# Performance work log

Hardware: AMD Instinct MI355X
Metric: run time of the kernel (lower is better)

Reference implementation:

```python
import jax, jax.numpy as jnp
import numpy as np

N = 100000
E = 1600000
F_NODE = 6
F_EDGE = 2
H = 64


def _glorot(key, shape):
    lim = float(np.sqrt(6.0 / (shape[0] + shape[1])))
    return jax.random.uniform(key, shape, jnp.float32, -lim, lim)


def setup_inputs() -> dict:
    key = jax.random.key(0)
    ks = jax.random.split(key, 16)
    inp = {
        "x": jax.random.normal(ks[0], (N, F_NODE), jnp.float32),
        "edge_index": jax.random.randint(ks[1], (2, E), 0, N, jnp.int64),
        "edge_attr": jax.random.normal(ks[2], (E, F_EDGE), jnp.float32),
        # GCN layers (PyG GCNConv: linear no-bias, then aggregate, then +bias)
        "W1": _glorot(ks[3], (F_NODE, H)), "b1": jnp.zeros((H,), jnp.float32),
        "W2": _glorot(ks[4], (H, H)), "b2": jnp.zeros((H,), jnp.float32),
        "W3": _glorot(ks[5], (H, H)), "b3": jnp.zeros((H,), jnp.float32),
        # edge_mlp
        "We1": _glorot(ks[6], (F_EDGE, H)), "be1": jnp.zeros((H,), jnp.float32),
        "We2": _glorot(ks[7], (H, H)), "be2": jnp.zeros((H,), jnp.float32),
        # predictor
        "Wp1": _glorot(ks[8], (3 * H, H)), "bp1": jnp.zeros((H,), jnp.float32),
        "Wp2": _glorot(ks[9], (H, H // 2)), "bp2": jnp.zeros((H // 2,), jnp.float32),
        "Wp3": _glorot(ks[10], (H // 2, 1)), "bp3": jnp.zeros((1,), jnp.float32),
    }
    return inp


def _gcn_conv(h, W, b, src_sl, dst_sl, norm, n):
    # PyG GCNConv with self-loops and symmetric normalization
    h = h @ W                                   # [N, H_out]
    msg = h[src_sl] * norm[:, None]             # gather + scale per edge(+loop)
    out = jax.ops.segment_sum(msg, dst_sl, num_segments=n)
    return out + b


def _forward(x, edge_attr, W1, b1, W2, b2, W3, b3, We1, be1, We2, be2,
             Wp1, bp1, Wp2, bp2, Wp3, bp3, edge_index):
    n = x.shape[0]
    src, dst = edge_index[0], edge_index[1]

    # --- edge feature injection (vectorized version of per-edge loop) ---
    ef = jax.nn.relu(edge_attr @ We1 + be1) @ We2 + be2      # [E, H]
    nef = (jax.ops.segment_sum(ef, src, num_segments=n)
           + jax.ops.segment_sum(ef, dst, num_segments=n))   # [N, H]
    ones_e = jnp.ones((ef.shape[0],), x.dtype)
    deg = (jax.ops.segment_sum(ones_e, src, num_segments=n)
           + jax.ops.segment_sum(ones_e, dst, num_segments=n))
    deg = jnp.maximum(deg, 1.0)
    nef = nef / deg[:, None]
    # hidden_dim (64) >= node feature dim (6) -> truncate
    x = x + nef[:, : x.shape[1]] * 0.5

    # --- GCN normalization with self-loops (shared across layers) ---
    loop = jnp.arange(n, dtype=src.dtype)
    src_sl = jnp.concatenate([src, loop])
    dst_sl = jnp.concatenate([dst, loop])
    deg_sl = jax.ops.segment_sum(jnp.ones_like(dst_sl, dtype=x.dtype), dst_sl,
                                 num_segments=n)
    dinv = jnp.where(deg_sl > 0, deg_sl ** -0.5, 0.0)
    norm = dinv[src_sl] * dinv[dst_sl]

    h = jax.nn.relu(_gcn_conv(x, W1, b1, src_sl, dst_sl, norm, n))
    h = jax.nn.relu(_gcn_conv(h, W2, b2, src_sl, dst_sl, norm, n))
    h = _gcn_conv(h, W3, b3, src_sl, dst_sl, norm, n)

    graph_emb = h.mean(axis=0)                 # global_mean_pool, batch=None
    node_mean = h.mean(axis=0)
    node_std = jnp.std(h, axis=0, ddof=1)      # torch.std is unbiased
    combined = jnp.concatenate([graph_emb, node_mean, node_std])  # [3H]

    p = jax.nn.relu(combined @ Wp1 + bp1)      # dropout inactive in eval
    p = jax.nn.relu(p @ Wp2 + bp2)
    out = jax.nn.sigmoid(p @ Wp3 + bp3)        # (1,)
    return out


def reference(x, edge_index, edge_attr, W1, b1, W2, b2, W3, b3,
              We1, be1, We2, be2, Wp1, bp1, Wp2, bp2, Wp3, bp3):
    return _forward(x, edge_attr, W1, b1, W2, b2, W3, b3, We1, be1, We2, be2,
                    Wp1, bp1, Wp2, bp2, Wp3, bp3, edge_index)
```

## Files before the change

kernel.cpp:

```cpp
#include <hip/hip_runtime.h>
#include <hip/hip_bf16.h>
#include <stdint.h>

typedef float floatx2 __attribute__((ext_vector_type(2)));

__device__ __forceinline__ float rdlane(float v, int l) {
    return __uint_as_float(__builtin_amdgcn_readlane(__float_as_uint(v), l));
}
__device__ __forceinline__ float bf2f(unsigned short u) {
    return __uint_as_float(((unsigned)u) << 16);
}
__device__ __forceinline__ unsigned short f2bf(float f) {
    unsigned u = __float_as_uint(f);
    u += 0x7fffu + ((u >> 16) & 1u);
    return (unsigned short)(u >> 16);
}
__device__ __forceinline__ unsigned packbf(float a, float b) {
    return (unsigned)f2bf(a) | ((unsigned)f2bf(b) << 16);
}
__device__ __forceinline__ unsigned pk_fp8x4(float a, float b, float c, float d) {
    int u = __builtin_amdgcn_cvt_pk_fp8_f32(a, b, 0, false);
    u = __builtin_amdgcn_cvt_pk_fp8_f32(c, d, u, true);
    return (unsigned)u;
}

__global__ void k_zero(int* __restrict__ cntO, int* __restrict__ cntI,
                       double* __restrict__ sums, int n) {
    int i = blockIdx.x * blockDim.x + threadIdx.x;
    if (i < 128) sums[i] = 0.0;
    if (i < n) { cntO[i] = 0; cntI[i] = 0; }
}

__global__ __launch_bounds__(256) void k_front(
    const int* __restrict__ ei, const float* __restrict__ ea,
    const float* __restrict__ We1, const float* __restrict__ be1,
    const float* __restrict__ We2, const float* __restrict__ be2,
    unsigned* __restrict__ efp, int* __restrict__ cntO, int* __restrict__ cntI,
    int* __restrict__ rankS, int* __restrict__ rankD, int E) {
    __shared__ float sWe1[128], sbe1[64], sWe2[64 * 6], sbe2[6];
    int t = threadIdx.x;
    if (t < 128) sWe1[t] = We1[t];
    if (t < 64) {
        sbe1[t] = be1[t];
#pragma unroll
        for (int c = 0; c < 6; ++c) sWe2[t * 6 + c] = We2[t * 64 + c];
    }
    if (t < 6) sbe2[t] = be2[t];
    __syncthreads();

    int e = blockIdx.x * blockDim.x + t;
    if (e >= E) return;

    int s = ei[e], d = ei[E + e];
    int rs = atomicAdd(&cntO[s], 1);
    int rd = atomicAdd(&cntI[d], 1);

    float2 aa = ((const float2*)ea)[e];
    float a0 = aa.x, a1 = aa.y;
    float acc[6];
#pragma unroll
    for (int c = 0; c < 6; ++c) acc[c] = sbe2[c];
#pragma unroll
    for (int j = 0; j < 64; ++j) {
        float h = fmaf(a0, sWe1[j], fmaf(a1, sWe1[64 + j], sbe1[j]));
        h = fmaxf(h, 0.f);
#pragma unroll
        for (int c = 0; c < 6; ++c) acc[c] = fmaf(h, sWe2[j * 6 + c], acc[c]);
    }
    unsigned* q = efp + (size_t)e * 3;
    q[0] = packbf(acc[0], acc[1]);
    q[1] = packbf(acc[2], acc[3]);
    q[2] = packbf(acc[4], acc[5]);
    rankS[e] = rs;
    rankD[e] = rd;
}

__global__ __launch_bounds__(256) void k_scan1(const int* __restrict__ cntO,
                                               const int* __restrict__ cntI,
                                               int2* __restrict__ bsum, int n) {
    __shared__ int2 l[256];
    int i = blockIdx.x * 256 + threadIdx.x;
    l[threadIdx.x] = (i < n) ? make_int2(cntO[i], cntI[i]) : make_int2(0, 0);
    __syncthreads();
    for (int s = 128; s > 0; s >>= 1) {
        if (threadIdx.x < s) {
            l[threadIdx.x].x += l[threadIdx.x + s].x;
            l[threadIdx.x].y += l[threadIdx.x + s].y;
        }
        __syncthreads();
    }
    if (threadIdx.x == 0) bsum[blockIdx.x] = l[0];
}

__global__ __launch_bounds__(512) void k_scan2(int2* __restrict__ bsum, int nb,
                                               int* __restrict__ offON,
                                               int* __restrict__ offIN) {
    __shared__ int2 l[512];
    int t = threadIdx.x;
    int2 v = (t < nb) ? bsum[t] : make_int2(0, 0);
    l[t] = v;
    __syncthreads();
    for (int s = 1; s < 512; s <<= 1) {
        int2 tmp = (t >= s) ? l[t - s] : make_int2(0, 0);
        __syncthreads();
        l[t].x += tmp.x; l[t].y += tmp.y;
        __syncthreads();
    }
    if (t < nb) bsum[t] = make_int2(l[t].x - v.x, l[t].y - v.y);
    if (t == 511) { *offON = l[511].x; *offIN = l[511].y; }
}

__global__ __launch_bounds__(256) void k_scan3off(const int* __restrict__ cntO,
                                                  const int* __restrict__ cntI,
                                                  const int2* __restrict__ bsum,
                                                  int* __restrict__ offO,
                                                  int* __restrict__ offI, int n) {
    __shared__ int2 l[256];
    int i = blockIdx.x * 256 + threadIdx.x;
    int2 v = (i < n) ? make_int2(cntO[i], cntI[i]) : make_int2(0, 0);
    l[threadIdx.x] = v;
    __syncthreads();
    for (int s = 1; s < 256; s <<= 1) {
        int2 tmp = (threadIdx.x >= (unsigned)s) ? l[threadIdx.x - s] : make_int2(0, 0);
        __syncthreads();
        l[threadIdx.x].x += tmp.x; l[threadIdx.x].y += tmp.y;
        __syncthreads();
    }
    if (i < n) {
        int2 bs = bsum[blockIdx.x];
        offO[i] = l[threadIdx.x].x - v.x + bs.x;
        offI[i] = l[threadIdx.x].y - v.y + bs.y;
    }
}

__global__ __launch_bounds__(256) void k_place(const int* __restrict__ ei,
                                               const int* __restrict__ rankS,
                                               const int* __restrict__ rankD,
                                               const int* __restrict__ offO,
                                               const int* __restrict__ offI,
                                               const unsigned* __restrict__ efp,
                                               unsigned* __restrict__ out_rec,
                                               uint4* __restrict__ in_rec, int E) {
    int e = blockIdx.x * blockDim.x + threadIdx.x;
    if (e >= E) return;
    int s = ei[e], d = ei[E + e];
    const unsigned* q = efp + (size_t)e * 3;
    unsigned u0 = q[0], u1 = q[1], u2 = q[2];
    size_t so = (size_t)(offO[s] + rankS[e]) * 3;
    out_rec[so] = u0; out_rec[so + 1] = u1; out_rec[so + 2] = u2;
    in_rec[offI[d] + rankD[e]] = make_uint4((unsigned)s, u0, u1, u2);
}

__global__ __launch_bounds__(256) void k_nef_x(
    const int* __restrict__ offO, const unsigned* __restrict__ out_rec,
    const int* __restrict__ offI, const uint4* __restrict__ in_rec,
    const float* __restrict__ x,
    float* __restrict__ xp, float* __restrict__ dinv, int n) {
    int i = blockIdx.x * blockDim.x + threadIdx.x;
    if (i >= n) return;
    int bo = offO[i], eo = offO[i + 1];
    int bi = offI[i], eiN = offI[i + 1];
    float a0 = 0.f, a1 = 0.f, a2 = 0.f, a3 = 0.f, a4 = 0.f, a5 = 0.f;
    for (int j = bo; j < eo; ++j) {
        const unsigned* q = out_rec + (size_t)j * 3;
        unsigned u0 = q[0], u1 = q[1], u2 = q[2];
        a0 += bf2f((unsigned short)u0); a1 += bf2f((unsigned short)(u0 >> 16));
        a2 += bf2f((unsigned short)u1); a3 += bf2f((unsigned short)(u1 >> 16));
        a4 += bf2f((unsigned short)u2); a5 += bf2f((unsigned short)(u2 >> 16));
    }
    for (int j = bi; j < eiN; ++j) {
        uint4 r = in_rec[j];
        a0 += bf2f((unsigned short)r.y); a1 += bf2f((unsigned short)(r.y >> 16));
        a2 += bf2f((unsigned short)r.z); a3 += bf2f((unsigned short)(r.z >> 16));
        a4 += bf2f((unsigned short)r.w); a5 += bf2f((unsigned short)(r.w >> 16));
    }
    int indeg = eiN - bi;
    float degf = (float)((eo - bo) + indeg);
    float inv = 0.5f / fmaxf(degf, 1.f);
    xp[(size_t)i * 6 + 0] = x[(size_t)i * 6 + 0] + a0 * inv;
    xp[(size_t)i * 6 + 1] = x[(size_t)i * 6 + 1] + a1 * inv;
    xp[(size_t)i * 6 + 2] = x[(size_t)i * 6 + 2] + a2 * inv;
    xp[(size_t)i * 6 + 3] = x[(size_t)i * 6 + 3] + a3 * inv;
    xp[(size_t)i * 6 + 4] = x[(size_t)i * 6 + 4] + a4 * inv;
    xp[(size_t)i * 6 + 5] = x[(size_t)i * 6 + 5] + a5 * inv;
    dinv[i] = 1.f / sqrtf(1.f + (float)indeg);
}

__global__ __launch_bounds__(256) void k_mm1(const float* __restrict__ xp,
                                             const float* __restrict__ W1,
                                             const float* __restrict__ dinv,
                                             unsigned* __restrict__ sOut, int n) {
    int lane = threadIdx.x & 63;
    int sub = lane & 15;
    int wid = (blockIdx.x * blockDim.x + threadIdx.x) >> 6;
    int nw = (gridDim.x * blockDim.x) >> 6;
    float w[6];
#pragma unroll
    for (int c = 0; c < 6; ++c) w[c] = W1[c * 64 + lane];
    for (int i = wid; i < n; i += nw) {
        float xv = (lane < 6) ? xp[(size_t)i * 6 + lane] : 0.f;
        float acc = 0.f;
#pragma unroll
        for (int c = 0; c < 6; ++c) acc = fmaf(rdlane(xv, c), w[c], acc);
        float o = acc * dinv[i];
        float o0 = __shfl(o, sub * 4 + 0);
        float o1 = __shfl(o, sub * 4 + 1);
        float o2 = __shfl(o, sub * 4 + 2);
        float o3 = __shfl(o, sub * 4 + 3);
        if (lane < 16) sOut[(size_t)i * 16 + lane] = pk_fp8x4(o0, o1, o2, o3);
    }
}

__global__ __launch_bounds__(256) void k_gathermm(
    const int* __restrict__ offI, const uint4* __restrict__ in_rec,
    const float* __restrict__ dinv, const unsigned* __restrict__ sIn,
    const float* __restrict__ bias, const float* __restrict__ W,
    unsigned* __restrict__ sOut, int n) {
    int lane = threadIdx.x & 63;
    int sub = lane & 15, grp = lane >> 4;
    int wid = (blockIdx.x * blockDim.x + threadIdx.x) >> 6;
    int nw = (gridDim.x * blockDim.x) >> 6;
    float w[64];
#pragma unroll
    for (int c = 0; c < 64; ++c) w[c] = W[c * 64 + lane];
    float4 bb = ((const float4*)bias)[sub];

    for (int i = wid; i < n; i += nw) {
        unsigned su = sIn[(size_t)i * 16 + sub];
        float a0, a1, a2, a3;
        if (grp == 0) {
            floatx2 lo = __builtin_amdgcn_cvt_pk_f32_fp8(su, false);
            floatx2 hi = __builtin_amdgcn_cvt_pk_f32_fp8(su, true);
            a0 = lo.x; a1 = lo.y; a2 = hi.x; a3 = hi.y;
        } else { a0 = a1 = a2 = a3 = 0.f; }
        int b0 = offI[i], e0 = offI[i + 1];
#pragma unroll 4
        for (int j = b0 + grp; j < e0; j += 4) {
            unsigned src = in_rec[j].x;
            unsigned u = sIn[(size_t)src * 16 + sub];
            floatx2 lo = __builtin_amdgcn_cvt_pk_f32_fp8(u, false);
            floatx2 hi = __builtin_amdgcn_cvt_pk_f32_fp8(u, true);
            a0 += lo.x; a1 += lo.y; a2 += hi.x; a3 += hi.y;
        }
        a0 += __shfl_xor(a0, 16); a1 += __shfl_xor(a1, 16);
        a2 += __shfl_xor(a2, 16); a3 += __shfl_xor(a3, 16);
        a0 += __shfl_xor(a0, 32); a1 += __shfl_xor(a1, 32);
        a2 += __shfl_xor(a2, 32); a3 += __shfl_xor(a3, 32);

        float dv = dinv[i];
        float h0 = fmaxf(fmaf(a0, dv, bb.x), 0.f);
        float h1 = fmaxf(fmaf(a1, dv, bb.y), 0.f);
        float h2 = fmaxf(fmaf(a2, dv, bb.z), 0.f);
        float h3 = fmaxf(fmaf(a3, dv, bb.w), 0.f);
        float o = 0.f;
#pragma unroll
        for (int g = 0; g < 16; ++g) {
            o = fmaf(rdlane(h0, g), w[g * 4 + 0], o);
            o = fmaf(rdlane(h1, g), w[g * 4 + 1], o);
            o = fmaf(rdlane(h2, g), w[g * 4 + 2], o);
            o = fmaf(rdlane(h3, g), w[g * 4 + 3], o);
        }
        o *= dv;
        float o0 = __shfl(o, sub * 4 + 0);
        float o1 = __shfl(o, sub * 4 + 1);
        float o2 = __shfl(o, sub * 4 + 2);
        float o3 = __shfl(o, sub * 4 + 3);
        if (lane < 16) sOut[(size_t)i * 16 + lane] = pk_fp8x4(o0, o1, o2, o3);
    }
}

__global__ __launch_bounds__(256) void k_gatherreduce(
    const int* __restrict__ offI, const uint4* __restrict__ in_rec,
    const float* __restrict__ dinv, const unsigned* __restrict__ sIn,
    const float* __restrict__ b3, double* __restrict__ sums, int n) {
    int lane = threadIdx.x & 63;
    int sub = lane & 15, grp = lane >> 4;
    int wv = threadIdx.x >> 6;
    int wid = (blockIdx.x * blockDim.x + threadIdx.x) >> 6;
    int nw = (gridDim.x * blockDim.x) >> 6;
    float4 bb = ((const float4*)b3)[sub];
    double s0 = 0.0, s1 = 0.0, s2_ = 0.0, s3 = 0.0;
    double q0 = 0.0, q1 = 0.0, q2 = 0.0, q3 = 0.0;

    for (int i = wid; i < n; i += nw) {
        unsigned su = sIn[(size_t)i * 16 + sub];
        float a0, a1, a2, a3;
        if (grp == 0) {
            floatx2 lo = __builtin_amdgcn_cvt_pk_f32_fp8(su, false);
            floatx2 hi = __builtin_amdgcn_cvt_pk_f32_fp8(su, true);
            a0 = lo.x; a1 = lo.y; a2 = hi.x; a3 = hi.y;
        } else { a0 = a1 = a2 = a3 = 0.f; }
        int b0 = offI[i], e0 = offI[i + 1];
#pragma unroll 4
        for (int j = b0 + grp; j < e0; j += 4) {
            unsigned src = in_rec[j].x;
            unsigned u = sIn[(size_t)src * 16 + sub];
            floatx2 lo = __builtin_amdgcn_cvt_pk_f32_fp8(u, false);
            floatx2 hi = __builtin_amdgcn_cvt_pk_f32_fp8(u, true);
            a0 += lo.x; a1 += lo.y; a2 += hi.x; a3 += hi.y;
        }
        a0 += __shfl_xor(a0, 16); a1 += __shfl_xor(a1, 16);
        a2 += __shfl_xor(a2, 16); a3 += __shfl_xor(a3, 16);
        a0 += __shfl_xor(a0, 32); a1 += __shfl_xor(a1, 32);
        a2 += __shfl_xor(a2, 32); a3 += __shfl_xor(a3, 32);

        float dv = dinv[i];
        float v0 = fmaf(a0, dv, bb.x);
        float v1 = fmaf(a1, dv, bb.y);
        float v2 = fmaf(a2, dv, bb.z);
        float v3 = fmaf(a3, dv, bb.w);
        s0 += v0; s1 += v1; s2_ += v2; s3 += v3;
        q0 += (double)v0 * v0; q1 += (double)v1 * v1;
        q2 += (double)v2 * v2; q3 += (double)v3 * v3;
    }
    __shared__ double shS[4 * 64], shQ[4 * 64];
    if (grp == 0) {
#pragma unroll
        for (int k = 0; k < 4; ++k) {
            double sk = (k == 0) ? s0 : (k == 1) ? s1 : (k == 2) ? s2_ : s3;
            double qk = (k == 0) ? q0 : (k == 1) ? q1 : (k == 2) ? q2 : q3;
            shS[wv * 64 + sub * 4 + k] = sk;
            shQ[wv * 64 + sub * 4 + k] = qk;
        }
    }
    __syncthreads();
    if (wv == 0) {
        double a = shS[lane] + shS[64 + lane] + shS[128 + lane] + shS[192 + lane];
        double c = shQ[lane] + shQ[64 + lane] + shQ[128 + lane] + shQ[192 + lane];
        unsafeAtomicAdd(&sums[lane], a);
        unsafeAtomicAdd(&sums[64 + lane], c);
    }
}

__global__ void k_head(const double* __restrict__ sums,
                       const float* __restrict__ Wp1, const float* __restrict__ bp1,
                       const float* __restrict__ Wp2, const float* __restrict__ bp2,
                       const float* __restrict__ Wp3, const float* __restrict__ bp3,
                       float* __restrict__ out, int n) {
    __shared__ float comb[192], p1[64], p2[32];
    int t = threadIdx.x;
    if (t < 64) {
        double s = sums[t], s2 = sums[64 + t];
        double m = s / n;
        double var = (s2 - s * s / n) / (double)(n - 1);
        float mf = (float)m;
        float sd = (float)sqrt(var > 0.0 ? var : 0.0);
        comb[t] = mf;
        comb[64 + t] = mf;
        comb[128 + t] = sd;
    }
    __syncthreads();
    if (t < 64) {
        float acc = bp1[t];
        for (int k = 0; k < 192; ++k) acc = fmaf(comb[k], Wp1[k * 64 + t], acc);
        p1[t] = fmaxf(acc, 0.f);
    }
    __syncthreads();
    if (t < 32) {
        float acc = bp2[t];
        for (int k = 0; k < 64; ++k) acc = fmaf(p1[k], Wp2[k * 32 + t], acc);
        p2[t] = fmaxf(acc, 0.f);
    }
    __syncthreads();
    if (t == 0) {
        float acc = bp3[0];
        for (int k = 0; k < 32; ++k) acc = fmaf(p2[k], Wp3[k], acc);
        out[0] = 1.f / (1.f + expf(-acc));
    }
}

static inline char* align16(char* p) {
    return (char*)(((uintptr_t)p + 15) & ~(uintptr_t)15);
}

extern "C" void kernel_launch(void* const* d_in, const int* in_sizes, int n_in,
                              void* d_out, int out_size, void* d_ws, size_t ws_size,
                              hipStream_t stream) {
    const float* x   = (const float*)d_in[0];
    const int*   ei  = (const int*)d_in[1];
    const float* ea  = (const float*)d_in[2];
    const float* W1  = (const float*)d_in[3];
    const float* b1  = (const float*)d_in[4];
    const float* W2  = (const float*)d_in[5];
    const float* b2  = (const float*)d_in[6];
    const float* W3  = (const float*)d_in[7];
    const float* b3  = (const float*)d_in[8];
    const float* We1 = (const float*)d_in[9];
    const float* be1 = (const float*)d_in[10];
    const float* We2 = (const float*)d_in[11];
    const float* be2 = (const float*)d_in[12];
    const float* Wp1 = (const float*)d_in[13];
    const float* bp1 = (const float*)d_in[14];
    const float* Wp2 = (const float*)d_in[15];
    const float* bp2 = (const float*)d_in[16];
    const float* Wp3 = (const float*)d_in[17];
    const float* bp3 = (const float*)d_in[18];

    const int N = in_sizes[0] / 6;
    const int E = in_sizes[1] / 2;
    const int nbN = (N + 255) / 256;
    const int nbE = (E + 255) / 256;
    const size_t SB = (size_t)N * 64;

    char* p = (char*)d_ws;
    double* sums = (double*)p;          p = align16(p + 128 * sizeof(double));
    int* cntO = (int*)p;                p = align16(p + (size_t)N * 4);
    int* cntI = (int*)p;                p = align16(p + (size_t)N * 4);
    int* offO = (int*)p;                p = align16(p + ((size_t)N + 1) * 4);
    int* offI = (int*)p;                p = align16(p + ((size_t)N + 1) * 4);
    int2* bsum = (int2*)p;              p = align16(p + 512 * 8);
    float* xp = (float*)p;              p = align16(p + (size_t)N * 6 * 4);
    float* dinv = (float*)p;            p = align16(p + (size_t)N * 4);
    uint4* in_rec = (uint4*)p;          p = align16(p + (size_t)E * 16);
    char* u1 = p;                       p = align16(p + 2 * ((SB + 15) & ~(size_t)15));
    int* rankS = (int*)u1;
    int* rankD = (int*)(u1 + ((SB + 15) & ~(size_t)15));
    unsigned* sbufA = (unsigned*)rankS;
    unsigned* sbufB = (unsigned*)rankD;
    char* u2 = p;
    unsigned* efp = (unsigned*)u2;
    unsigned* out_rec = (unsigned*)(u2 + (size_t)E * 12);

    const int TB = 256;
    dim3 blk(TB);

    k_zero<<<dim3(nbN), blk, 0, stream>>>(cntO, cntI, sums, N);
    k_front<<<dim3(nbE), blk, 0, stream>>>(ei, ea, We1, be1, We2, be2,
                                           efp, cntO, cntI, rankS, rankD, E);
    k_scan1<<<dim3(nbN), blk, 0, stream>>>(cntO, cntI, bsum, N);
    k_scan2<<<dim3(1), dim3(512), 0, stream>>>(bsum, nbN, offO + N, offI + N);
    k_scan3off<<<dim3(nbN), blk, 0, stream>>>(cntO, cntI, bsum, offO, offI, N);
    k_place<<<dim3(nbE), blk, 0, stream>>>(ei, rankS, rankD, offO, offI, efp,
                                           out_rec, in_rec, E);
    k_nef_x<<<dim3(nbN), blk, 0, stream>>>(offO, out_rec, offI, in_rec, x, xp, dinv, N);

    k_mm1<<<dim3(1024), blk, 0, stream>>>(xp, W1, dinv, sbufA, N);
    k_gathermm<<<dim3(2048), blk, 0, stream>>>(offI, in_rec, dinv, sbufA, b1, W2, sbufB, N);
    k_gathermm<<<dim3(2048), blk, 0, stream>>>(offI, in_rec, dinv, sbufB, b2, W3, sbufA, N);
    k_gatherreduce<<<dim3(2048), blk, 0, stream>>>(offI, in_rec, dinv, sbufA, b3, sums, N);
    k_head<<<dim3(1), dim3(64), 0, stream>>>(sums, Wp1, bp1, Wp2, bp2, Wp3, bp3,
                                             (float*)d_out, N);
}
```

Baseline: 543.8 us.

## Store edge features as fp8, fuse nef with mm1, compact source index array

Edge MLP outputs are packed as fp8 into 8-byte records instead of bf16 12-byte ones, shrinking the placement and aggregation traffic. The node edge-feature aggregation kernel now also computes the first GCN linear layer, removing the xp buffer and one launch. It also writes a compact 4-byte source-index array that the three gather kernels read instead of 16-byte in_rec entries. Nontemporal loads and stores are used on streaming data. The change lowers precision on edge features and adds a write of the index array.

```diff
diff --git a/kernel.cpp b/kernel.cpp
--- a/kernel.cpp
+++ b/kernel.cpp
@@ -3,25 +3,18 @@
 #include <stdint.h>
 
 typedef float floatx2 __attribute__((ext_vector_type(2)));
+typedef unsigned uint32x4 __attribute__((ext_vector_type(4)));
 
 __device__ __forceinline__ float rdlane(float v, int l) {
     return __uint_as_float(__builtin_amdgcn_readlane(__float_as_uint(v), l));
-}
-__device__ __forceinline__ float bf2f(unsigned short u) {
-    return __uint_as_float(((unsigned)u) << 16);
-}
-__device__ __forceinline__ unsigned short f2bf(float f) {
-    unsigned u = __float_as_uint(f);
-    u += 0x7fffu + ((u >> 16) & 1u);
-    return (unsigned short)(u >> 16);
-}
-__device__ __forceinline__ unsigned packbf(float a, float b) {
-    return (unsigned)f2bf(a) | ((unsigned)f2bf(b) << 16);
 }
 __device__ __forceinline__ unsigned pk_fp8x4(float a, float b, float c, float d) {
     int u = __builtin_amdgcn_cvt_pk_fp8_f32(a, b, 0, false);
     u = __builtin_amdgcn_cvt_pk_fp8_f32(c, d, u, true);
     return (unsigned)u;
+}
+__device__ __forceinline__ unsigned pk_fp8x2(float a, float b) {
+    return (unsigned)__builtin_amdgcn_cvt_pk_fp8_f32(a, b, 0, false);
 }
 
 __global__ void k_zero(int* __restrict__ cntO, int* __restrict__ cntI,
@@ -35,7 +28,7 @@
     const int* __restrict__ ei, const float* __restrict__ ea,
     const float* __restrict__ We1, const float* __restrict__ be1,
     const float* __restrict__ We2, const float* __restrict__ be2,
-    unsigned* __restrict__ efp, int* __restrict__ cntO, int* __restrict__ cntI,
+    uint2* __restrict__ efp, int* __restrict__ cntO, int* __restrict__ cntI,
     int* __restrict__ rankS, int* __restrict__ rankD, int E) {
     __shared__ float sWe1[128], sbe1[64], sWe2[64 * 6], sbe2[6];
     int t = threadIdx.x;
@@ -56,21 +49,18 @@
     int rd = atomicAdd(&cntI[d], 1);
 
     float2 aa = ((const float2*)ea)[e];
-    float a0 = aa.x, a1 = aa.y;
     float acc[6];
 #pragma unroll
     for (int c = 0; c < 6; ++c) acc[c] = sbe2[c];
 #pragma unroll
     for (int j = 0; j < 64; ++j) {
-        float h = fmaf(a0, sWe1[j], fmaf(a1, sWe1[64 + j], sbe1[j]));
+        float h = fmaf(aa.x, sWe1[j], fmaf(aa.y, sWe1[64 + j], sbe1[j]));
         h = fmaxf(h, 0.f);
 #pragma unroll
         for (int c = 0; c < 6; ++c) acc[c] = fmaf(h, sWe2[j * 6 + c], acc[c]);
     }
-    unsigned* q = efp + (size_t)e * 3;
-    q[0] = packbf(acc[0], acc[1]);
-    q[1] = packbf(acc[2], acc[3]);
-    q[2] = packbf(acc[4], acc[5]);
+    efp[e] = make_uint2(pk_fp8x4(acc[0], acc[1], acc[2], acc[3]),
+                        pk_fp8x2(acc[4], acc[5]));
     rankS[e] = rs;
     rankD[e] = rd;
 }
@@ -91,7 +81,6 @@
     }
     if (threadIdx.x == 0) bsum[blockIdx.x] = l[0];
 }
-
 __global__ __launch_bounds__(512) void k_scan2(int2* __restrict__ bsum, int nb,
                                                int* __restrict__ offON,
                                                int* __restrict__ offIN) {
@@ -109,7 +98,6 @@
     if (t < nb) bsum[t] = make_int2(l[t].x - v.x, l[t].y - v.y);
     if (t == 511) { *offON = l[511].x; *offIN = l[511].y; }
 }
-
 __global__ __launch_bounds__(256) void k_scan3off(const int* __restrict__ cntO,
                                                   const int* __restrict__ cntI,
                                                   const int2* __restrict__ bsum,
@@ -138,81 +126,83 @@
                                                const int* __restrict__ rankD,
                                                const int* __restrict__ offO,
                                                const int* __restrict__ offI,
-                                               const unsigned* __restrict__ efp,
-                                               unsigned* __restrict__ out_rec,
+                                               const uint2* __restrict__ efp,
+                                               uint2* __restrict__ out_rec,
                                                uint4* __restrict__ in_rec, int E) {
     int e = blockIdx.x * blockDim.x + threadIdx.x;
     if (e >= E) return;
     int s = ei[e], d = ei[E + e];
-    const unsigned* q = efp + (size_t)e * 3;
-    unsigned u0 = q[0], u1 = q[1], u2 = q[2];
-    size_t so = (size_t)(offO[s] + rankS[e]) * 3;
-    out_rec[so] = u0; out_rec[so + 1] = u1; out_rec[so + 2] = u2;
-    in_rec[offI[d] + rankD[e]] = make_uint4((unsigned)s, u0, u1, u2);
-}
-
-__global__ __launch_bounds__(256) void k_nef_x(
-    const int* __restrict__ offO, const unsigned* __restrict__ out_rec,
+    uint2 f = efp[e];
+    out_rec[offO[s] + rankS[e]] = f;
+    in_rec[offI[d] + rankD[e]] = make_uint4((unsigned)s, f.x, f.y, 0u);
+}
+
+__global__ __launch_bounds__(256) void k_nefmm1(
+    const int* __restrict__ offO, const uint2* __restrict__ out_rec,
     const int* __restrict__ offI, const uint4* __restrict__ in_rec,
-    const float* __restrict__ x,
-    float* __restrict__ xp, float* __restrict__ dinv, int n) {
-    int i = blockIdx.x * blockDim.x + threadIdx.x;
+    const float* __restrict__ x, const float* __restrict__ W1,
+    float* __restrict__ dinv, int* __restrict__ in_src,
+    unsigned* __restrict__ sOut, int n) {
+    __shared__ float sW1[384];
+    int t = threadIdx.x;
+    for (int idx = t; idx < 384; idx += 256) sW1[idx] = W1[idx];
+    __syncthreads();
+
+    int i = blockIdx.x * blockDim.x + t;
     if (i >= n) return;
     int bo = offO[i], eo = offO[i + 1];
     int bi = offI[i], eiN = offI[i + 1];
     float a0 = 0.f, a1 = 0.f, a2 = 0.f, a3 = 0.f, a4 = 0.f, a5 = 0.f;
     for (int j = bo; j < eo; ++j) {
-        const unsigned* q = out_rec + (size_t)j * 3;
-        unsigned u0 = q[0], u1 = q[1], u2 = q[2];
-        a0 += bf2f((unsigned short)u0); a1 += bf2f((unsigned short)(u0 >> 16));
-        a2 += bf2f((unsigned short)u1); a3 += bf2f((unsigned short)(u1 >> 16));
-        a4 += bf2f((unsigned short)u2); a5 += bf2f((unsigned short)(u2 >> 16));
+        uint2 q = out_rec[j];
+        floatx2 p01 = __builtin_amdgcn_cvt_pk_f32_fp8(q.x, false);
+        floatx2 p23 = __builtin_amdgcn_cvt_pk_f32_fp8(q.x, true);
+        floatx2 p45 = __builtin_amdgcn_cvt_pk_f32_fp8(q.y, false);
+        a0 += p01.x; a1 += p01.y; a2 += p23.x;
+        a3 += p23.y; a4 += p45.x; a5 += p45.y;
     }
     for (int j = bi; j < eiN; ++j) {
         uint4 r = in_rec[j];
-        a0 += bf2f((unsigned short)r.y); a1 += bf2f((unsigned short)(r.y >> 16));
-        a2 += bf2f((unsigned short)r.z); a3 += bf2f((unsigned short)(r.z >> 16));
-        a4 += bf2f((unsigned short)r.w); a5 += bf2f((unsigned short)(r.w >> 16));
+        __builtin_nontemporal_store((int)r.x, in_src + j);
+        floatx2 p01 = __builtin_amdgcn_cvt_pk_f32_fp8(r.y, false);
+        floatx2 p23 = __builtin_amdgcn_cvt_pk_f32_fp8(r.y, true);
+        floatx2 p45 = __builtin_amdgcn_cvt_pk_f32_fp8(r.z, false);
+        a0 += p01.x; a1 += p01.y; a2 += p23.x;
+        a3 += p23.y; a4 += p45.x; a5 += p45.y;
     }
     int indeg = eiN - bi;
     float degf = (float)((eo - bo) + indeg);
     float inv = 0.5f / fmaxf(degf, 1.f);
-    xp[(size_t)i * 6 + 0] = x[(size_t)i * 6 + 0] + a0 * inv;
-    xp[(size_t)i * 6 + 1] = x[(size_t)i * 6 + 1] + a1 * inv;
-    xp[(size_t)i * 6 + 2] = x[(size_t)i * 6 + 2] + a2 * inv;
-    xp[(size_t)i * 6 + 3] = x[(size_t)i * 6 + 3] + a3 * inv;
-    xp[(size_t)i * 6 + 4] = x[(size_t)i * 6 + 4] + a4 * inv;
-    xp[(size_t)i * 6 + 5] = x[(size_t)i * 6 + 5] + a5 * inv;
-    dinv[i] = 1.f / sqrtf(1.f + (float)indeg);
-}
-
-__global__ __launch_bounds__(256) void k_mm1(const float* __restrict__ xp,
-                                             const float* __restrict__ W1,
-                                             const float* __restrict__ dinv,
-                                             unsigned* __restrict__ sOut, int n) {
-    int lane = threadIdx.x & 63;
-    int sub = lane & 15;
-    int wid = (blockIdx.x * blockDim.x + threadIdx.x) >> 6;
-    int nw = (gridDim.x * blockDim.x) >> 6;
-    float w[6];
-#pragma unroll
-    for (int c = 0; c < 6; ++c) w[c] = W1[c * 64 + lane];
-    for (int i = wid; i < n; i += nw) {
-        float xv = (lane < 6) ? xp[(size_t)i * 6 + lane] : 0.f;
-        float acc = 0.f;
-#pragma unroll
-        for (int c = 0; c < 6; ++c) acc = fmaf(rdlane(xv, c), w[c], acc);
-        float o = acc * dinv[i];
-        float o0 = __shfl(o, sub * 4 + 0);
-        float o1 = __shfl(o, sub * 4 + 1);
-        float o2 = __shfl(o, sub * 4 + 2);
-        float o3 = __shfl(o, sub * 4 + 3);
-        if (lane < 16) sOut[(size_t)i * 16 + lane] = pk_fp8x4(o0, o1, o2, o3);
+    const float2* xr = (const float2*)(x + (size_t)i * 6);
+    float2 x01 = xr[0], x23 = xr[1], x45 = xr[2];
+    float xp0 = x01.x + a0 * inv, xp1 = x01.y + a1 * inv;
+    float xp2 = x23.x + a2 * inv, xp3 = x23.y + a3 * inv;
+    float xp4 = x45.x + a4 * inv, xp5 = x45.y + a5 * inv;
+    float dv = 1.f / sqrtf(1.f + (float)indeg);
+    dinv[i] = dv;
+
+    unsigned u[16];
+#pragma unroll
+    for (int c4 = 0; c4 < 16; ++c4) {
+        float tv[4];
+#pragma unroll
+        for (int k = 0; k < 4; ++k) {
+            int c = c4 * 4 + k;
+            float v = xp0 * sW1[c] + xp1 * sW1[64 + c] + xp2 * sW1[128 + c]
+                    + xp3 * sW1[192 + c] + xp4 * sW1[256 + c] + xp5 * sW1[320 + c];
+            tv[k] = v * dv;
+        }
+        u[c4] = pk_fp8x4(tv[0], tv[1], tv[2], tv[3]);
+    }
+#pragma unroll
+    for (int q4 = 0; q4 < 4; ++q4) {
+        uint32x4 v = {u[q4 * 4 + 0], u[q4 * 4 + 1], u[q4 * 4 + 2], u[q4 * 4 + 3]};
+        __builtin_nontemporal_store(v, (uint32x4*)(sOut + (size_t)i * 16) + q4);
     }
 }
 
 __global__ __launch_bounds__(256) void k_gathermm(
-    const int* __restrict__ offI, const uint4* __restrict__ in_rec,
+    const int* __restrict__ offI, const int* __restrict__ in_src,
     const float* __restrict__ dinv, const unsigned* __restrict__ sIn,
     const float* __restrict__ bias, const float* __restrict__ W,
     unsigned* __restrict__ sOut, int n) {
@@ -236,7 +226,7 @@
         int b0 = offI[i], e0 = offI[i + 1];
 #pragma unroll 4
         for (int j = b0 + grp; j < e0; j += 4) {
-            unsigned src = in_rec[j].x;
+            unsigned src = (unsigned)__builtin_nontemporal_load(in_src + j);
             unsigned u = sIn[(size_t)src * 16 + sub];
             floatx2 lo = __builtin_amdgcn_cvt_pk_f32_fp8(u, false);
             floatx2 hi = __builtin_amdgcn_cvt_pk_f32_fp8(u, true);
@@ -265,12 +255,14 @@
         float o1 = __shfl(o, sub * 4 + 1);
         float o2 = __shfl(o, sub * 4 + 2);
         float o3 = __shfl(o, sub * 4 + 3);
-        if (lane < 16) sOut[(size_t)i * 16 + lane] = pk_fp8x4(o0, o1, o2, o3);
+        if (lane < 16)
+            __builtin_nontemporal_store(pk_fp8x4(o0, o1, o2, o3),
+                                        sOut + (size_t)i * 16 + lane);
     }
 }
 
 __global__ __launch_bounds__(256) void k_gatherreduce(
-    const int* __restrict__ offI, const uint4* __restrict__ in_rec,
+    const int* __restrict__ offI, const int* __restrict__ in_src,
     const float* __restrict__ dinv, const unsigned* __restrict__ sIn,
     const float* __restrict__ b3, double* __restrict__ sums, int n) {
     int lane = threadIdx.x & 63;
@@ -293,7 +285,7 @@
         int b0 = offI[i], e0 = offI[i + 1];
 #pragma unroll 4
         for (int j = b0 + grp; j < e0; j += 4) {
-            unsigned src = in_rec[j].x;
+            unsigned src = (unsigned)__builtin_nontemporal_load(in_src + j);
             unsigned u = sIn[(size_t)src * 16 + sub];
             floatx2 lo = __builtin_amdgcn_cvt_pk_f32_fp8(u, false);
             floatx2 hi = __builtin_amdgcn_cvt_pk_f32_fp8(u, true);
@@ -400,7 +392,7 @@
     const int E = in_sizes[1] / 2;
     const int nbN = (N + 255) / 256;
     const int nbE = (E + 255) / 256;
-    const size_t SB = (size_t)N * 64;
+    const size_t SB = ((size_t)N * 64 + 15) & ~(size_t)15;
 
     char* p = (char*)d_ws;
     double* sums = (double*)p;          p = align16(p + 128 * sizeof(double));
@@ -409,20 +401,19 @@
     int* offO = (int*)p;                p = align16(p + ((size_t)N + 1) * 4);
     int* offI = (int*)p;                p = align16(p + ((size_t)N + 1) * 4);
     int2* bsum = (int2*)p;              p = align16(p + 512 * 8);
-    float* xp = (float*)p;              p = align16(p + (size_t)N * 6 * 4);
     float* dinv = (float*)p;            p = align16(p + (size_t)N * 4);
+    int* in_src = (int*)p;              p = align16(p + (size_t)E * 4);
     uint4* in_rec = (uint4*)p;          p = align16(p + (size_t)E * 16);
-    char* u1 = p;                       p = align16(p + 2 * ((SB + 15) & ~(size_t)15));
+    char* u1 = p;                       p = align16(p + 2 * SB);
     int* rankS = (int*)u1;
-    int* rankD = (int*)(u1 + ((SB + 15) & ~(size_t)15));
-    unsigned* sbufA = (unsigned*)rankS;
-    unsigned* sbufB = (unsigned*)rankD;
+    int* rankD = (int*)(u1 + SB);
+    unsigned* sbufA = (unsigned*)u1;
+    unsigned* sbufB = (unsigned*)(u1 + SB);
     char* u2 = p;
-    unsigned* efp = (unsigned*)u2;
-    unsigned* out_rec = (unsigned*)(u2 + (size_t)E * 12);
-
-    const int TB = 256;
-    dim3 blk(TB);
+    uint2* efp = (uint2*)u2;
+    uint2* out_rec = (uint2*)(u2 + (size_t)E * 8);
+
+    dim3 blk(256);
 
     k_zero<<<dim3(nbN), blk, 0, stream>>>(cntO, cntI, sums, N);
     k_front<<<dim3(nbE), blk, 0, stream>>>(ei, ea, We1, be1, We2, be2,
@@ -432,12 +423,12 @@
     k_scan3off<<<dim3(nbN), blk, 0, stream>>>(cntO, cntI, bsum, offO, offI, N);
     k_place<<<dim3(nbE), blk, 0, stream>>>(ei, rankS, rankD, offO, offI, efp,
                                            out_rec, in_rec, E);
-    k_nef_x<<<dim3(nbN), blk, 0, stream>>>(offO, out_rec, offI, in_rec, x, xp, dinv, N);
-
-    k_mm1<<<dim3(1024), blk, 0, stream>>>(xp, W1, dinv, sbufA, N);
-    k_gathermm<<<dim3(2048), blk, 0, stream>>>(offI, in_rec, dinv, sbufA, b1, W2, sbufB, N);
-    k_gathermm<<<dim3(2048), blk, 0, stream>>>(offI, in_rec, dinv, sbufB, b2, W3, sbufA, N);
-    k_gatherreduce<<<dim3(2048), blk, 0, stream>>>(offI, in_rec, dinv, sbufA, b3, sums, N);
+    k_nefmm1<<<dim3(nbN), blk, 0, stream>>>(offO, out_rec, offI, in_rec, x, W1,
+                                            dinv, in_src, sbufA, N);
+
+    k_gathermm<<<dim3(2048), blk, 0, stream>>>(offI, in_src, dinv, sbufA, b1, W2, sbufB, N);
+    k_gathermm<<<dim3(2048), blk, 0, stream>>>(offI, in_src, dinv, sbufB, b2, W3, sbufA, N);
+    k_gatherreduce<<<dim3(2048), blk, 0, stream>>>(offI, in_src, dinv, sbufA, b3, sums, N);
     k_head<<<dim3(1), dim3(64), 0, stream>>>(sums, Wp1, bp1, Wp2, bp2, Wp3, bp3,
                                              (float*)d_out, N);
 }
```

Measured after the change: 603.0 us (median of 2 runs). +10.9%, slower.
